# Kernel tuning notes

Measured on AMD Instinct MI355X. Metric: run time of the kernel, lower is better.

Reference implementation:

```python
import jax, jax.numpy as jnp
import numpy as np

NUM_HEADS = 16
NUM_KV_HEADS = 8
HEAD_DIM = 128
HIDDEN = 2048
Q_SIZE = NUM_HEADS * HEAD_DIM          # 2048
KV_SIZE = NUM_KV_HEADS * HEAD_DIM      # 1024
SCALING = 256.0 ** -0.5                # query_pre_attn_scalar ** -0.5
EPS = 1e-6
BATCH = 8
ENC_LEN = 512                          # encoder_len_per_req
Q_LEN = 2048                           # sum of extend_seq_lens (8 * 256)
KV_LEN = BATCH * ENC_LEN               # 4096


def _rms_norm(x, w):
    # Gemma3RMSNorm: fp32 compute, scale by (1 + weight)
    xf = x.astype(jnp.float32)
    xf = xf * jax.lax.rsqrt(jnp.mean(xf * xf, axis=-1, keepdims=True) + EPS)
    return (xf * (1.0 + w.astype(jnp.float32))).astype(x.dtype)


def setup_inputs() -> dict:
    key = jax.random.key(0)
    k1, k2, k3 = jax.random.split(key, 3)
    return {
        "hidden_states": jax.random.normal(k1, (Q_LEN, HIDDEN), jnp.float32),
        "encoder_hidden_states": jax.random.normal(k2, (KV_LEN, HIDDEN), jnp.float32),
        "w_qkv": jax.random.normal(k3, (Q_SIZE + 2 * KV_SIZE, HIDDEN), jnp.float32) * 0.02,
        "q_norm_w": jnp.zeros((HEAD_DIM,), jnp.float32),
        "k_norm_w": jnp.zeros((HEAD_DIM,), jnp.float32),
        "seq_lens": jnp.full((BATCH,), Q_LEN // BATCH, jnp.int32),  # extend_seq_lens per request
    }


def reference(hidden_states, encoder_hidden_states, w_qkv, q_norm_w, k_norm_w, seq_lens):
    # decoder side: only q is used
    qkv_dec = hidden_states @ w_qkv.T                     # [q_len, 4096]
    q = qkv_dec[:, :Q_SIZE].reshape(Q_LEN, NUM_HEADS, HEAD_DIM)
    q = _rms_norm(q, q_norm_w) * SCALING

    # encoder side: only k, v are used
    qkv_enc = encoder_hidden_states @ w_qkv.T             # [kv_len, 4096]
    k = qkv_enc[:, Q_SIZE:Q_SIZE + KV_SIZE].reshape(KV_LEN, NUM_KV_HEADS, HEAD_DIM)
    v = qkv_enc[:, Q_SIZE + KV_SIZE:].reshape(KV_LEN, NUM_KV_HEADS, HEAD_DIM)
    k = _rms_norm(k, k_norm_w)

    # GQA: repeat each kv head n_rep times (consecutively, matching expand+reshape)
    n_rep = NUM_HEADS // NUM_KV_HEADS
    k = jnp.repeat(k, n_rep, axis=1)                      # [kv_len, H, D]
    v = jnp.repeat(v, n_rep, axis=1)

    # scores per head: [H, q_len, kv_len]
    scores = jnp.einsum('qhd,khd->hqk', q, k)

    # ragged block-diagonal mask: query token i belongs to request r iff
    # cumsum(seq_lens)[r-1] <= i < cumsum(seq_lens)[r]; kv token j -> j // ENC_LEN
    q_req = jnp.searchsorted(jnp.cumsum(seq_lens), jnp.arange(Q_LEN), side='right')
    kv_req = jnp.arange(KV_LEN) // ENC_LEN
    mask = q_req[:, None] == kv_req[None, :]              # [q_len, kv_len] bool
    scores = jnp.where(mask[None, :, :], scores, -jnp.inf)

    attn = jax.nn.softmax(scores.astype(jnp.float32), axis=-1).astype(v.dtype)
    out = jnp.einsum('hqk,khd->qhd', attn, v)             # [q_len, H, D]
    return out.reshape(Q_LEN, NUM_HEADS * HEAD_DIM)
```

## Files before the change

### kernel.cpp

```cpp
#include <hip/hip_runtime.h>

typedef __attribute__((ext_vector_type(8))) short short8;
typedef __attribute__((ext_vector_type(4))) float f32x4;

#define DEVI __device__ __forceinline__

static constexpr int HIDDEN   = 2048;
static constexpr int NHEADS   = 16;
static constexpr int NKV      = 8;
static constexpr int HDIM     = 128;
static constexpr int QLEN     = 2048;
static constexpr int KVLEN    = 4096;
static constexpr int ENCLEN   = 512;
static constexpr int NREQ     = 8;
static constexpr float SCALING = 0.0625f;
static constexpr float EPS     = 1e-6f;

DEVI unsigned short f2bf(float f) {
  unsigned int b = __float_as_uint(f);
  b += 0x7FFFu + ((b >> 16) & 1u);
  return (unsigned short)(b >> 16);
}

DEVI void g2l16(const void* g, void* l) {
  __builtin_amdgcn_global_load_lds(
      (const __attribute__((address_space(1))) void*)g,
      (__attribute__((address_space(3))) void*)l, 16, 0, 0);
}

__global__ __launch_bounds__(256) void cvt_all(const float* __restrict__ h,
                                               const float* __restrict__ e,
                                               const float* __restrict__ w,
                                               unsigned short* __restrict__ hb,
                                               unsigned short* __restrict__ eb,
                                               unsigned short* __restrict__ wb) {
  constexpr long S1 = (long)2048 * 2048, S2 = (long)4096 * 2048;
  long i = ((long)blockIdx.x * 256 + threadIdx.x) * 8;
  const float* src;
  unsigned short* dst;
  if (i < S1)           { src = h + i;            dst = hb + i; }
  else if (i < S1 + S2) { src = e + (i - S1);     dst = eb + (i - S1); }
  else                  { src = w + (i - S1 - S2); dst = wb + (i - S1 - S2); }
  float4 a = *(const float4*)src;
  float4 b = *(const float4*)(src + 4);
  short8 o;
  o[0] = (short)f2bf(a.x); o[1] = (short)f2bf(a.y);
  o[2] = (short)f2bf(a.z); o[3] = (short)f2bf(a.w);
  o[4] = (short)f2bf(b.x); o[5] = (short)f2bf(b.y);
  o[6] = (short)f2bf(b.z); o[7] = (short)f2bf(b.w);
  *(short8*)dst = o;
}


#define LGKM0 { asm volatile("s_waitcnt lgkmcnt(0)" ::: "memory"); __builtin_amdgcn_sched_barrier(0); }
#define VM8   { asm volatile("s_waitcnt vmcnt(8)" ::: "memory"); __builtin_amdgcn_sched_barrier(0); }
#define VM4   { asm volatile("s_waitcnt vmcnt(4)" ::: "memory"); __builtin_amdgcn_sched_barrier(0); }
#define VM0   { asm volatile("s_waitcnt vmcnt(0)" ::: "memory"); __builtin_amdgcn_sched_barrier(0); }
#define SBAR  __builtin_amdgcn_s_barrier()

DEVI short8 rdfrag(const char* unit, int row, int lg) {
  int L = row >> 1;
  int g = ((row & 1) << 2) + lg;
  return *(const short8*)(unit + L * 128 + ((g ^ (L & 7)) << 4));
}

__global__ __launch_bounds__(512, 2) void gemm_qkv8(
    const unsigned short* __restrict__ Adec, const unsigned short* __restrict__ Aenc,
    const unsigned short* __restrict__ Bw,
    const float* __restrict__ q_nw, const float* __restrict__ k_nw,
    unsigned short* __restrict__ q_bf, unsigned short* __restrict__ k_bf,
    unsigned short* __restrict__ v_t) {
  extern __shared__ char lds[];
  const int K = 2048, NT = 32;

  int flat = blockIdx.y * 8 + blockIdx.x;
  int swz = (flat & 7) * 24 + (flat >> 3);
  int bx = swz & 7, by = swz >> 3;

  const unsigned short* A;
  int bm0;
  if (by < 8) { A = Adec; bm0 = by * 256; }
  else        { A = Aenc; bm0 = (by - 8) * 256; }
  const unsigned short* Bp = Bw + (by < 8 ? 0 : (size_t)2048 * 2048);
  const int bn0 = bx * 256;

  const int tid = threadIdx.x, lane = tid & 63, wave = tid >> 6;
  const int lr = lane & 15, lg = lane >> 4;
  const int wr = wave >> 2, wc = wave & 3;
  const int bq = (wc & 1) * 64;

#define SLOT(kt, kk) ((((kt) << 1) | (kk)) & 3)
#define AUs(s, h) (lds + ((((s) << 1) | (h)) << 13))
#define BUs(s, h) (lds + 65536 + ((((s) << 1) | (h)) << 13))

  const int sB = tid * 16;
  const int sL = sB >> 7, sgp = (sB >> 4) & 7;
  const int sg = sgp ^ (sL & 7);
  const int st_row = sL * 2 + (sg >> 2);
  const int st_col = (sg & 3) * 8;
  const size_t a0off = (size_t)(bm0 + st_row) * K + st_col;
  const size_t a1off = a0off + (size_t)128 * K;
  const size_t b0off = (size_t)(bn0 + st_row) * K + st_col;
  const size_t b1off = b0off + (size_t)128 * K;

#define STG(srcp, ubase) g2l16((srcp), (ubase) + sB)
#define STG4(kt, kk)                                                \
  {                                                                 \
    const size_t kc = (size_t)(kt) * 64 + (kk) * 32;                \
    const int s_ = SLOT(kt, kk);                                    \
    STG(A + a0off + kc, AUs(s_, 0));  STG(A + a1off + kc, AUs(s_, 1)); \
    STG(Bp + b0off + kc, BUs(s_, 0)); STG(Bp + b1off + kc, BUs(s_, 1)); \
  }

  f32x4 acc[8][4] = {};
  short8 a[4], b[4];

#define DS_A(s, mq)                                                 \
  {                                                                 \
    const char* u = AUs(s, wr);                                     \
    _Pragma("unroll") for (int m = 0; m < 4; ++m)                   \
        a[m] = rdfrag(u, (mq)*64 + m * 16 + lr, lg);                \
  }
#define DS_B(s)                                                     \
  {                                                                 \
    const char* u = BUs(s, wc >> 1);                                \
    _Pragma("unroll") for (int n = 0; n < 4; ++n)                   \
        b[n] = rdfrag(u, bq + n * 16 + lr, lg);                     \
  }
#define MFMA16(mq)                                                  \
  {                                                                 \
    __builtin_amdgcn_s_setprio(1);                                  \
    _Pragma("unroll") for (int m = 0; m < 4; ++m)                   \
        _Pragma("unroll") for (int n = 0; n < 4; ++n)               \
            acc[(mq)*4 + m][n] = __builtin_amdgcn_mfma_f32_16x16x32_bf16( \
                a[m], b[n], acc[(mq)*4 + m][n], 0, 0, 0);           \
    __builtin_amdgcn_s_setprio(0);                                  \
  }

  STG4(0, 0); STG4(0, 1); STG4(1, 0);
  VM8; SBAR;

  for (int kt = 0; kt < NT - 2; ++kt) {
    const int s0 = SLOT(kt, 0), s1 = SLOT(kt, 1);
    DS_A(s0, 0); DS_B(s0); STG4(kt + 1, 1); LGKM0; MFMA16(0); SBAR;
    DS_A(s0, 1);                            LGKM0; MFMA16(1); VM8; SBAR;
    DS_A(s1, 0); DS_B(s1); STG4(kt + 2, 0); LGKM0; MFMA16(0); SBAR;
    DS_A(s1, 1);                            LGKM0; MFMA16(1); VM8; SBAR;
  }
  {
    const int s0 = SLOT(NT - 2, 0), s1 = SLOT(NT - 2, 1);
    DS_A(s0, 0); DS_B(s0); STG4(NT - 1, 1); LGKM0; MFMA16(0); SBAR;
    DS_A(s0, 1);                            LGKM0; MFMA16(1); VM8; SBAR;
    DS_A(s1, 0); DS_B(s1);                  LGKM0; MFMA16(0); SBAR;
    DS_A(s1, 1);                            LGKM0; MFMA16(1); VM4; SBAR;
  }
  {
    const int s0 = SLOT(NT - 1, 0), s1 = SLOT(NT - 1, 1);
    DS_A(s0, 0); DS_B(s0); LGKM0; MFMA16(0); SBAR;
    DS_A(s0, 1);           LGKM0; MFMA16(1); VM0; SBAR;
    DS_A(s1, 0); DS_B(s1); LGKM0; MFMA16(0); SBAR;
    DS_A(s1, 1);           LGKM0; MFMA16(1);
  }

  const int btype = (by < 8) ? 0 : (bx < 4 ? 1 : 2);
  const int tokbase0 = (by < 8 ? by : by - 8) * 256;

  if (btype < 2) {
    float* Lf = (float*)lds;
    const float* wnorm = (btype == 0) ? q_nw : k_nw;
    const float fscale = (btype == 0) ? SCALING : 1.0f;
    unsigned short* dst = (btype == 0) ? q_bf : k_bf;
    const size_t LEN = (btype == 0) ? (size_t)QLEN : (size_t)KVLEN;
    const int dloc = lr * 8;
    float wv[8];
#pragma unroll
    for (int j = 0; j < 8; ++j) wv[j] = 1.0f + wnorm[dloc + j];

#pragma unroll
    for (int q = 0; q < 4; ++q) {
      SBAR;
      if (wr == (q >> 1)) {
        const int amb = (q & 1) * 4;
#pragma unroll
        for (int am2 = 0; am2 < 4; ++am2)
#pragma unroll
          for (int n = 0; n < 4; ++n)
#pragma unroll
            for (int r = 0; r < 4; ++r)
              Lf[(am2 * 16 + lg * 4 + r) * 260 + wc * 64 + n * 16 + lr] =
                  acc[amb + am2][n][r];
      }
      SBAR;
#pragma unroll
      for (int it = 0; it < 4; ++it) {
        int pair = it * 32 + wave * 4 + (lane >> 4);
        int row = pair >> 1, hh = pair & 1;
        const float* src = &Lf[row * 260 + hh * 128 + dloc];
        f32x4 x0 = *(const f32x4*)src;
        f32x4 x1 = *(const f32x4*)(src + 4);
        float ssq = x0[0]*x0[0] + x0[1]*x0[1] + x0[2]*x0[2] + x0[3]*x0[3] +
                    x1[0]*x1[0] + x1[1]*x1[1] + x1[2]*x1[2] + x1[3]*x1[3];
#pragma unroll
        for (int m = 8; m >= 1; m >>= 1) ssq += __shfl_xor(ssq, m);
        float sc = rsqrtf(ssq * (1.0f / 128.0f) + EPS) * fscale;
        short8 o;
        o[0] = (short)f2bf(x0[0] * sc * wv[0]); o[1] = (short)f2bf(x0[1] * sc * wv[1]);
        o[2] = (short)f2bf(x0[2] * sc * wv[2]); o[3] = (short)f2bf(x0[3] * sc * wv[3]);
        o[4] = (short)f2bf(x1[0] * sc * wv[4]); o[5] = (short)f2bf(x1[1] * sc * wv[5]);
        o[6] = (short)f2bf(x1[2] * sc * wv[6]); o[7] = (short)f2bf(x1[3] * sc * wv[7]);
        int tok = tokbase0 + q * 64 + row;
        int hd = 2 * bx + hh;
        *(short8*)&dst[((size_t)hd * LEN + tok) * 128 + dloc] = o;
      }
    }
  } else {
    float* Lv = (float*)lds;
#pragma unroll
    for (int q = 0; q < 4; ++q) {
      SBAR;
      if (wr == (q >> 1)) {
        const int amb = (q & 1) * 4;
#pragma unroll
        for (int am2 = 0; am2 < 4; ++am2)
#pragma unroll
          for (int n = 0; n < 4; ++n)
            *(f32x4*)&Lv[(wc * 64 + n * 16 + lr) * 68 + am2 * 16 + lg * 4] =
                acc[amb + am2][n];
      }
      SBAR;
      int d = tid >> 1, th = tid & 1;
      const float* src = &Lv[d * 68 + th * 32];
      int kh = (bx - 4) * 2 + (d >> 7);
      int tok = tokbase0 + q * 64 + th * 32;
      unsigned short* vp = &v_t[((size_t)kh * 128 + (d & 127)) * KVLEN + tok];
#pragma unroll
      for (int j = 0; j < 4; ++j) {
        f32x4 v0 = *(const f32x4*)(src + j * 8);
        f32x4 v1 = *(const f32x4*)(src + j * 8 + 4);
        short8 o;
        o[0] = (short)f2bf(v0[0]); o[1] = (short)f2bf(v0[1]);
        o[2] = (short)f2bf(v0[2]); o[3] = (short)f2bf(v0[3]);
        o[4] = (short)f2bf(v1[0]); o[5] = (short)f2bf(v1[1]);
        o[6] = (short)f2bf(v1[2]); o[7] = (short)f2bf(v1[3]);
        *(short8*)(vp + j * 8) = o;
      }
    }
  }
#undef SLOT
#undef AUs
#undef BUs
#undef STG
#undef STG4
#undef DS_A
#undef DS_B
#undef MFMA16
}

__global__ __launch_bounds__(256, 4) void attn_kernel(
    const unsigned short* __restrict__ qb,
    const unsigned short* __restrict__ kb,
    const unsigned short* __restrict__ vt,
    const int* __restrict__ seq_lens,
    float* __restrict__ out) {
  __shared__ __align__(16) unsigned short Ks[64 * 128];
  __shared__ __align__(16) unsigned short Vs[128 * 64];
  __shared__ __align__(16) unsigned short Ps[64 * 64];

  const int h = blockIdx.y;
  const int t0 = blockIdx.x * 64;
  int req = 0, qs = 0;
#pragma unroll 1
  while (req < NREQ - 1 && qs + seq_lens[req] <= t0) { qs += seq_lens[req]; ++req; }
  const int slen = seq_lens[req];
  const int rows = min(64, qs + slen - t0);
  if (rows <= 0) return;
  const int qbase = t0;

  const int tid = threadIdx.x, lane = tid & 63, wave = tid >> 6;
  const int lr = lane & 15, lg = lane >> 4;
  const int m0w = wave * 16;
  const int kh = h >> 1;
  const int kv0 = req * ENCLEN;

  short8 a_q[4];
  {
    int qr = qbase + min(m0w + lr, rows - 1);
    const unsigned short* qp = qb + ((size_t)h * QLEN + qr) * 128 + lg * 8;
#pragma unroll
    for (int ks = 0; ks < 4; ++ks) a_q[ks] = *(const short8*)(qp + ks * 32);
  }

  f32x4 acc[8] = {};
  float mrow[4], lsum[4];
#pragma unroll
  for (int r = 0; r < 4; ++r) { mrow[r] = -1e30f; lsum[r] = 0.f; }

  for (int c = 0; c < 8; ++c) {
#pragma unroll
    for (int i = 0; i < 4; ++i) {
      int idx = i * 256 + tid;
      int row = idx >> 4, slot = idx & 15;
      g2l16(kb + ((size_t)kh * KVLEN + kv0 + c * 64 + row) * 128 + ((slot ^ (row & 15)) << 3),
            &Ks[idx * 8]);
    }
#pragma unroll
    for (int i = 0; i < 4; ++i) {
      int idx = i * 256 + tid;
      int row = idx >> 3, slot = idx & 7;
      g2l16(vt + ((size_t)kh * 128 + row) * KVLEN + kv0 + c * 64 + ((slot ^ (row & 7)) << 3),
            &Vs[idx * 8]);
    }
    __syncthreads();

    f32x4 s[4] = {};
#pragma unroll
    for (int ks = 0; ks < 4; ++ks) {
      short8 bk[4];
#pragma unroll
      for (int n = 0; n < 4; ++n) {
        int row = n * 16 + lr;
        bk[n] = *(const short8*)&Ks[row * 128 + (((ks * 4 + lg) ^ (row & 15)) << 3)];
      }
#pragma unroll
      for (int n = 0; n < 4; ++n)
        s[n] = __builtin_amdgcn_mfma_f32_16x16x32_bf16(a_q[ks], bk[n], s[n], 0, 0, 0);
    }

#pragma unroll
    for (int r = 0; r < 4; ++r) {
      float mx = fmaxf(fmaxf(s[0][r], s[1][r]), fmaxf(s[2][r], s[3][r]));
#pragma unroll
      for (int msk = 8; msk >= 1; msk >>= 1) mx = fmaxf(mx, __shfl_xor(mx, msk));
      float mnew = fmaxf(mrow[r], mx);
      float al = __expf(mrow[r] - mnew);
      mrow[r] = mnew;
      float rs = 0.f;
#pragma unroll
      for (int n = 0; n < 4; ++n) {
        float p = __expf(s[n][r] - mnew);
        s[n][r] = p;
        rs += p;
      }
#pragma unroll
      for (int msk = 8; msk >= 1; msk >>= 1) rs += __shfl_xor(rs, msk);
      lsum[r] = lsum[r] * al + rs;
#pragma unroll
      for (int n2 = 0; n2 < 8; ++n2) acc[n2][r] *= al;
    }

#pragma unroll
    for (int n = 0; n < 4; ++n)
#pragma unroll
      for (int r = 0; r < 4; ++r) {
        int row = m0w + lg * 4 + r;
        int col = n * 16 + lr;
        Ps[row * 64 + (col ^ ((row & 7) << 3))] = f2bf(s[n][r]);
      }
    asm volatile("s_waitcnt lgkmcnt(0)" ::: "memory");
    __builtin_amdgcn_sched_barrier(0);

#pragma unroll
    for (int ks = 0; ks < 2; ++ks) {
      int prow = m0w + lr;
      short8 pa = *(const short8*)&Ps[prow * 64 + (((ks * 4 + lg) ^ (prow & 7)) << 3)];
#pragma unroll
      for (int n2 = 0; n2 < 8; ++n2) {
        int row = n2 * 16 + lr;
        short8 bv = *(const short8*)&Vs[row * 64 + (((ks * 4 + lg) ^ (row & 7)) << 3)];
        acc[n2] = __builtin_amdgcn_mfma_f32_16x16x32_bf16(pa, bv, acc[n2], 0, 0, 0);
      }
    }
    __syncthreads();
  }

  float inv[4];
#pragma unroll
  for (int r = 0; r < 4; ++r) inv[r] = 1.0f / lsum[r];
#pragma unroll
  for (int n2 = 0; n2 < 8; ++n2)
#pragma unroll
    for (int r = 0; r < 4; ++r) acc[n2][r] *= inv[r];

  constexpr int OFS = 132;
  float* Of = (float*)Ks;
#pragma unroll
  for (int n2 = 0; n2 < 8; ++n2)
#pragma unroll
    for (int r = 0; r < 4; ++r)
      Of[(m0w + lg * 4 + r) * OFS + n2 * 16 + lr] = acc[n2][r];
  __syncthreads();
#pragma unroll
  for (int p = 0; p < 8; ++p) {
    int idx = p * 256 + tid;
    int row = idx >> 5, c4 = (idx & 31) * 4;
    if (row < rows) {
      f32x4 v = *(const f32x4*)&Of[row * OFS + c4];
      *(f32x4*)&out[(size_t)(qbase + row) * 2048 + h * 128 + c4] = v;
    }
  }
}

extern "C" void kernel_launch(void* const* d_in, const int* in_sizes, int n_in,
                              void* d_out, int out_size, void* d_ws, size_t ws_size,
                              hipStream_t stream) {
  const float* hidden = (const float*)d_in[0];
  const float* enc    = (const float*)d_in[1];
  const float* w_qkv  = (const float*)d_in[2];
  const float* q_nw   = (const float*)d_in[3];
  const float* k_nw   = (const float*)d_in[4];
  const int*   slens  = (const int*)d_in[5];
  float* out = (float*)d_out;

  char* ws = (char*)d_ws;
  unsigned short* h_bf = (unsigned short*)(ws + 0);
  unsigned short* e_bf = (unsigned short*)(ws + 8388608);
  unsigned short* w_bf = (unsigned short*)(ws + 25165824);
  unsigned short* q_bf = (unsigned short*)(ws + 41943040);
  unsigned short* k_bf = (unsigned short*)(ws + 50331648);
  unsigned short* v_t  = (unsigned short*)(ws + 58720256);

  static bool attr_set = false;
  if (!attr_set) {
    hipFuncSetAttribute((const void*)gemm_qkv8,
                        hipFuncAttributeMaxDynamicSharedMemorySize, 131072);
    attr_set = true;
  }

  cvt_all<<<10240, 256, 0, stream>>>(hidden, enc, w_qkv, h_bf, e_bf, w_bf);

  gemm_qkv8<<<dim3(8, 24), 512, 131072, stream>>>(h_bf, e_bf, w_bf, q_nw, k_nw,
                                                  q_bf, k_bf, v_t);

  attn_kernel<<<dim3(32, 16), 256, 0, stream>>>(q_bf, k_bf, v_t, slens, out);
}
```

Before: 116.2 us.

## Double-buffer LDS fragment registers to overlap ds_reads with MFMA in QKV GEMM

Restructures the QKV GEMM main loop so the LDS fragment loads for the next MFMA group go into alternate register sets (aE/aO, bX/bY) while the current group's MFMAs run. The explicit lgkmcnt(0) waits and sched barriers are removed, leaving the compiler to insert LDS waits. The goal is to hide LDS read latency behind matrix math. In exchange it uses more VGPRs under a 512-thread, 2-block launch bound, which may cause spills, and the vmcnt waits now sit before the LDS reads.

```diff
diff --git a/kernel.cpp b/kernel.cpp
--- a/kernel.cpp
+++ b/kernel.cpp
@@ -52,10 +52,9 @@
 }
 
 
-#define LGKM0 { asm volatile("s_waitcnt lgkmcnt(0)" ::: "memory"); __builtin_amdgcn_sched_barrier(0); }
-#define VM8   { asm volatile("s_waitcnt vmcnt(8)" ::: "memory"); __builtin_amdgcn_sched_barrier(0); }
-#define VM4   { asm volatile("s_waitcnt vmcnt(4)" ::: "memory"); __builtin_amdgcn_sched_barrier(0); }
-#define VM0   { asm volatile("s_waitcnt vmcnt(0)" ::: "memory"); __builtin_amdgcn_sched_barrier(0); }
+#define VM8   { asm volatile("s_waitcnt vmcnt(8)" ::: "memory"); }
+#define VM4   { asm volatile("s_waitcnt vmcnt(4)" ::: "memory"); }
+#define VM0   { asm volatile("s_waitcnt vmcnt(0)" ::: "memory"); }
 #define SBAR  __builtin_amdgcn_s_barrier()
 
 DEVI short8 rdfrag(const char* unit, int row, int lg) {
@@ -113,53 +112,58 @@
   }
 
   f32x4 acc[8][4] = {};
-  short8 a[4], b[4];
-
-#define DS_A(s, mq)                                                 \
+  short8 aE[4], aO[4], bX[4], bY[4];
+
+#define LDA(dst, s, mq)                                             \
   {                                                                 \
     const char* u = AUs(s, wr);                                     \
     _Pragma("unroll") for (int m = 0; m < 4; ++m)                   \
-        a[m] = rdfrag(u, (mq)*64 + m * 16 + lr, lg);                \
-  }
-#define DS_B(s)                                                     \
+        dst[m] = rdfrag(u, (mq)*64 + m * 16 + lr, lg);              \
+  }
+#define LDB(dst, s)                                                 \
   {                                                                 \
     const char* u = BUs(s, wc >> 1);                                \
     _Pragma("unroll") for (int n = 0; n < 4; ++n)                   \
-        b[n] = rdfrag(u, bq + n * 16 + lr, lg);                     \
-  }
-#define MFMA16(mq)                                                  \
+        dst[n] = rdfrag(u, bq + n * 16 + lr, lg);                   \
+  }
+#define MM(mq, aS, bS)                                              \
   {                                                                 \
     __builtin_amdgcn_s_setprio(1);                                  \
     _Pragma("unroll") for (int m = 0; m < 4; ++m)                   \
         _Pragma("unroll") for (int n = 0; n < 4; ++n)               \
             acc[(mq)*4 + m][n] = __builtin_amdgcn_mfma_f32_16x16x32_bf16( \
-                a[m], b[n], acc[(mq)*4 + m][n], 0, 0, 0);           \
+                aS[m], bS[n], acc[(mq)*4 + m][n], 0, 0, 0);         \
     __builtin_amdgcn_s_setprio(0);                                  \
   }
 
   STG4(0, 0); STG4(0, 1); STG4(1, 0);
   VM8; SBAR;
+  LDA(aE, SLOT(0, 0), 0);
+  LDB(bX, SLOT(0, 0));
 
   for (int kt = 0; kt < NT - 2; ++kt) {
     const int s0 = SLOT(kt, 0), s1 = SLOT(kt, 1);
-    DS_A(s0, 0); DS_B(s0); STG4(kt + 1, 1); LGKM0; MFMA16(0); SBAR;
-    DS_A(s0, 1);                            LGKM0; MFMA16(1); VM8; SBAR;
-    DS_A(s1, 0); DS_B(s1); STG4(kt + 2, 0); LGKM0; MFMA16(0); SBAR;
-    DS_A(s1, 1);                            LGKM0; MFMA16(1); VM8; SBAR;
+    VM8; LDA(aO, s0, 1); STG4(kt + 1, 1);            MM(0, aE, bX); SBAR;
+    VM8; LDA(aE, s1, 0); LDB(bY, s1);                MM(1, aO, bX); SBAR;
+    VM8; LDA(aO, s1, 1); STG4(kt + 2, 0);            MM(0, aE, bY); SBAR;
+    VM8; LDA(aE, SLOT(kt + 1, 0), 0);
+         LDB(bX, SLOT(kt + 1, 0));                   MM(1, aO, bY); SBAR;
   }
   {
-    const int s0 = SLOT(NT - 2, 0), s1 = SLOT(NT - 2, 1);
-    DS_A(s0, 0); DS_B(s0); STG4(NT - 1, 1); LGKM0; MFMA16(0); SBAR;
-    DS_A(s0, 1);                            LGKM0; MFMA16(1); VM8; SBAR;
-    DS_A(s1, 0); DS_B(s1);                  LGKM0; MFMA16(0); SBAR;
-    DS_A(s1, 1);                            LGKM0; MFMA16(1); VM4; SBAR;
+    const int kt = NT - 2;
+    const int s0 = SLOT(kt, 0), s1 = SLOT(kt, 1);
+    VM8; LDA(aO, s0, 1); STG4(NT - 1, 1);            MM(0, aE, bX); SBAR;
+    VM8; LDA(aE, s1, 0); LDB(bY, s1);                MM(1, aO, bX); SBAR;
+    VM8; LDA(aO, s1, 1);                             MM(0, aE, bY); SBAR;
+    VM4; LDA(aE, SLOT(NT - 1, 0), 0);
+         LDB(bX, SLOT(NT - 1, 0));                   MM(1, aO, bY); SBAR;
   }
   {
     const int s0 = SLOT(NT - 1, 0), s1 = SLOT(NT - 1, 1);
-    DS_A(s0, 0); DS_B(s0); LGKM0; MFMA16(0); SBAR;
-    DS_A(s0, 1);           LGKM0; MFMA16(1); VM0; SBAR;
-    DS_A(s1, 0); DS_B(s1); LGKM0; MFMA16(0); SBAR;
-    DS_A(s1, 1);           LGKM0; MFMA16(1);
+    VM4; LDA(aO, s0, 1);                             MM(0, aE, bX); SBAR;
+    VM0; LDA(aE, s1, 0); LDB(bY, s1);                MM(1, aO, bX); SBAR;
+         LDA(aO, s1, 1);                             MM(0, aE, bY); SBAR;
+                                                     MM(1, aO, bY);
   }
 
   const int btype = (by < 8) ? 0 : (bx < 4 ? 1 : 2);
@@ -251,9 +255,9 @@
 #undef BUs
 #undef STG
 #undef STG4
-#undef DS_A
-#undef DS_B
-#undef MFMA16
+#undef LDA
+#undef LDB
+#undef MM
 }
 
 __global__ __launch_bounds__(256, 4) void attn_kernel(
```

Result: no change. 114.8 us (-1.2%).

## Restructure GEMM into 3-stage ring pipeline and double-buffer attention K/V loads

Applied to the files above, without the earlier changes.

The QKV GEMM main loop drops the 4-slot, two-half-step schedule with explicit lgkm/vm waits. It becomes a simpler 3-buffer ring over 32-wide k-steps, with one barrier per step and prefetch two steps ahead. The attention kernel now double-buffers the K and V tiles in shared memory, so the next chunk's global-to-LDS loads overlap the current chunk's compute, and one barrier per iteration is removed. The cost is more LDS in attention (72KB), which may cut occupancy from 4 blocks per CU. The GEMM also loses its fine-grained wait placement and now does twice as many barrier steps.

```diff
diff --git a/kernel.cpp b/kernel.cpp
--- a/kernel.cpp
+++ b/kernel.cpp
@@ -52,10 +52,6 @@
 }
 
 
-#define LGKM0 { asm volatile("s_waitcnt lgkmcnt(0)" ::: "memory"); __builtin_amdgcn_sched_barrier(0); }
-#define VM8   { asm volatile("s_waitcnt vmcnt(8)" ::: "memory"); __builtin_amdgcn_sched_barrier(0); }
-#define VM4   { asm volatile("s_waitcnt vmcnt(4)" ::: "memory"); __builtin_amdgcn_sched_barrier(0); }
-#define VM0   { asm volatile("s_waitcnt vmcnt(0)" ::: "memory"); __builtin_amdgcn_sched_barrier(0); }
 #define SBAR  __builtin_amdgcn_s_barrier()
 
 DEVI short8 rdfrag(const char* unit, int row, int lg) {
@@ -71,7 +67,7 @@
     unsigned short* __restrict__ q_bf, unsigned short* __restrict__ k_bf,
     unsigned short* __restrict__ v_t) {
   extern __shared__ char lds[];
-  const int K = 2048, NT = 32;
+  const int K = 2048, NST = 64;
 
   int flat = blockIdx.y * 8 + blockIdx.x;
   int swz = (flat & 7) * 24 + (flat >> 3);
@@ -88,10 +84,6 @@
   const int lr = lane & 15, lg = lane >> 4;
   const int wr = wave >> 2, wc = wave & 3;
   const int bq = (wc & 1) * 64;
-
-#define SLOT(kt, kk) ((((kt) << 1) | (kk)) & 3)
-#define AUs(s, h) (lds + ((((s) << 1) | (h)) << 13))
-#define BUs(s, h) (lds + 65536 + ((((s) << 1) | (h)) << 13))
 
   const int sB = tid * 16;
   const int sL = sB >> 7, sgp = (sB >> 4) & 7;
@@ -103,63 +95,61 @@
   const size_t b0off = (size_t)(bn0 + st_row) * K + st_col;
   const size_t b1off = b0off + (size_t)128 * K;
 
-#define STG(srcp, ubase) g2l16((srcp), (ubase) + sB)
-#define STG4(kt, kk)                                                \
-  {                                                                 \
-    const size_t kc = (size_t)(kt) * 64 + (kk) * 32;                \
-    const int s_ = SLOT(kt, kk);                                    \
-    STG(A + a0off + kc, AUs(s_, 0));  STG(A + a1off + kc, AUs(s_, 1)); \
-    STG(Bp + b0off + kc, BUs(s_, 0)); STG(Bp + b1off + kc, BUs(s_, 1)); \
+#define STG4(t)                                                       \
+  {                                                                   \
+    const size_t kc = (size_t)(t) * 32;                               \
+    char* base = lds + ((t) % 3) * 32768;                             \
+    g2l16(A + a0off + kc,  base + sB);                                \
+    g2l16(A + a1off + kc,  base + 8192 + sB);                         \
+    g2l16(Bp + b0off + kc, base + 16384 + sB);                        \
+    g2l16(Bp + b1off + kc, base + 24576 + sB);                        \
   }
 
   f32x4 acc[8][4] = {};
-  short8 a[4], b[4];
-
-#define DS_A(s, mq)                                                 \
-  {                                                                 \
-    const char* u = AUs(s, wr);                                     \
-    _Pragma("unroll") for (int m = 0; m < 4; ++m)                   \
-        a[m] = rdfrag(u, (mq)*64 + m * 16 + lr, lg);                \
-  }
-#define DS_B(s)                                                     \
-  {                                                                 \
-    const char* u = BUs(s, wc >> 1);                                \
-    _Pragma("unroll") for (int n = 0; n < 4; ++n)                   \
-        b[n] = rdfrag(u, bq + n * 16 + lr, lg);                     \
-  }
-#define MFMA16(mq)                                                  \
-  {                                                                 \
-    __builtin_amdgcn_s_setprio(1);                                  \
-    _Pragma("unroll") for (int m = 0; m < 4; ++m)                   \
-        _Pragma("unroll") for (int n = 0; n < 4; ++n)               \
+
+#define MM(mq, aS, bS)                                                \
+  {                                                                   \
+    __builtin_amdgcn_s_setprio(1);                                    \
+    _Pragma("unroll") for (int m = 0; m < 4; ++m)                     \
+        _Pragma("unroll") for (int n = 0; n < 4; ++n)                 \
             acc[(mq)*4 + m][n] = __builtin_amdgcn_mfma_f32_16x16x32_bf16( \
-                a[m], b[n], acc[(mq)*4 + m][n], 0, 0, 0);           \
-    __builtin_amdgcn_s_setprio(0);                                  \
-  }
-
-  STG4(0, 0); STG4(0, 1); STG4(1, 0);
-  VM8; SBAR;
-
-  for (int kt = 0; kt < NT - 2; ++kt) {
-    const int s0 = SLOT(kt, 0), s1 = SLOT(kt, 1);
-    DS_A(s0, 0); DS_B(s0); STG4(kt + 1, 1); LGKM0; MFMA16(0); SBAR;
-    DS_A(s0, 1);                            LGKM0; MFMA16(1); VM8; SBAR;
-    DS_A(s1, 0); DS_B(s1); STG4(kt + 2, 0); LGKM0; MFMA16(0); SBAR;
-    DS_A(s1, 1);                            LGKM0; MFMA16(1); VM8; SBAR;
+                aS[m], bS[n], acc[(mq)*4 + m][n], 0, 0, 0);           \
+    __builtin_amdgcn_s_setprio(0);                                    \
+  }
+
+  STG4(0); STG4(1);
+
+#pragma unroll 3
+  for (int t = 0; t < NST - 1; ++t) {
+    asm volatile("s_waitcnt vmcnt(4)" ::: "memory");
+    SBAR;
+    const char* ua = lds + (t % 3) * 32768 + wr * 8192;
+    const char* ub = lds + (t % 3) * 32768 + 16384 + ((wc >> 1) << 13);
+    short8 a0[4], b0[4], a1[4];
+#pragma unroll
+    for (int m = 0; m < 4; ++m) a0[m] = rdfrag(ua, m * 16 + lr, lg);
+#pragma unroll
+    for (int n = 0; n < 4; ++n) b0[n] = rdfrag(ub, bq + n * 16 + lr, lg);
+    if (t < NST - 2) STG4(t + 2);
+    MM(0, a0, b0);
+#pragma unroll
+    for (int m = 0; m < 4; ++m) a1[m] = rdfrag(ua, 64 + m * 16 + lr, lg);
+    MM(1, a1, b0);
   }
   {
-    const int s0 = SLOT(NT - 2, 0), s1 = SLOT(NT - 2, 1);
-    DS_A(s0, 0); DS_B(s0); STG4(NT - 1, 1); LGKM0; MFMA16(0); SBAR;
-    DS_A(s0, 1);                            LGKM0; MFMA16(1); VM8; SBAR;
-    DS_A(s1, 0); DS_B(s1);                  LGKM0; MFMA16(0); SBAR;
-    DS_A(s1, 1);                            LGKM0; MFMA16(1); VM4; SBAR;
-  }
-  {
-    const int s0 = SLOT(NT - 1, 0), s1 = SLOT(NT - 1, 1);
-    DS_A(s0, 0); DS_B(s0); LGKM0; MFMA16(0); SBAR;
-    DS_A(s0, 1);           LGKM0; MFMA16(1); VM0; SBAR;
-    DS_A(s1, 0); DS_B(s1); LGKM0; MFMA16(0); SBAR;
-    DS_A(s1, 1);           LGKM0; MFMA16(1);
+    asm volatile("s_waitcnt vmcnt(0)" ::: "memory");
+    SBAR;
+    const char* ua = lds + ((NST - 1) % 3) * 32768 + wr * 8192;
+    const char* ub = lds + ((NST - 1) % 3) * 32768 + 16384 + ((wc >> 1) << 13);
+    short8 a0[4], b0[4], a1[4];
+#pragma unroll
+    for (int m = 0; m < 4; ++m) a0[m] = rdfrag(ua, m * 16 + lr, lg);
+#pragma unroll
+    for (int n = 0; n < 4; ++n) b0[n] = rdfrag(ub, bq + n * 16 + lr, lg);
+    MM(0, a0, b0);
+#pragma unroll
+    for (int m = 0; m < 4; ++m) a1[m] = rdfrag(ua, 64 + m * 16 + lr, lg);
+    MM(1, a1, b0);
   }
 
   const int btype = (by < 8) ? 0 : (bx < 4 ? 1 : 2);
@@ -246,14 +236,8 @@
       }
     }
   }
-#undef SLOT
-#undef AUs
-#undef BUs
-#undef STG
 #undef STG4
-#undef DS_A
-#undef DS_B
-#undef MFMA16
+#undef MM
 }
 
 __global__ __launch_bounds__(256, 4) void attn_kernel(
@@ -262,9 +246,7 @@
     const unsigned short* __restrict__ vt,
     const int* __restrict__ seq_lens,
     float* __restrict__ out) {
-  __shared__ __align__(16) unsigned short Ks[64 * 128];
-  __shared__ __align__(16) unsigned short Vs[128 * 64];
-  __shared__ __align__(16) unsigned short Ps[64 * 64];
+  __shared__ __align__(16) char smem[73728];
 
   const int h = blockIdx.y;
   const int t0 = blockIdx.x * 64;
@@ -282,6 +264,25 @@
   const int kh = h >> 1;
   const int kv0 = req * ENCLEN;
 
+#define STAGE_K(c, db)                                                        \
+  _Pragma("unroll") for (int i = 0; i < 4; ++i) {                             \
+    int idx = i * 256 + tid;                                                  \
+    int row = idx >> 4, slot = idx & 15;                                      \
+    g2l16(kb + ((size_t)kh * KVLEN + kv0 + (c) * 64 + row) * 128 +            \
+              ((slot ^ (row & 15)) << 3),                                     \
+          smem + (db) * 16384 + idx * 16);                                    \
+  }
+#define STAGE_V(c, db)                                                        \
+  _Pragma("unroll") for (int i = 0; i < 4; ++i) {                             \
+    int idx = i * 256 + tid;                                                  \
+    int row = idx >> 3, slot = idx & 7;                                       \
+    g2l16(vt + ((size_t)kh * 128 + row) * KVLEN + kv0 + (c) * 64 +            \
+              ((slot ^ (row & 7)) << 3),                                      \
+          smem + 32768 + (db) * 16384 + idx * 16);                            \
+  }
+
+  unsigned short* Ps = (unsigned short*)(smem + 65536);
+
   short8 a_q[4];
   {
     int qr = qbase + min(m0w + lr, rows - 1);
@@ -295,22 +296,16 @@
 #pragma unroll
   for (int r = 0; r < 4; ++r) { mrow[r] = -1e30f; lsum[r] = 0.f; }
 
+  STAGE_K(0, 0); STAGE_V(0, 0);
+
+  int cb = 0;
+#pragma unroll 1
   for (int c = 0; c < 8; ++c) {
-#pragma unroll
-    for (int i = 0; i < 4; ++i) {
-      int idx = i * 256 + tid;
-      int row = idx >> 4, slot = idx & 15;
-      g2l16(kb + ((size_t)kh * KVLEN + kv0 + c * 64 + row) * 128 + ((slot ^ (row & 15)) << 3),
-            &Ks[idx * 8]);
-    }
-#pragma unroll
-    for (int i = 0; i < 4; ++i) {
-      int idx = i * 256 + tid;
-      int row = idx >> 3, slot = idx & 7;
-      g2l16(vt + ((size_t)kh * 128 + row) * KVLEN + kv0 + c * 64 + ((slot ^ (row & 7)) << 3),
-            &Vs[idx * 8]);
-    }
+    asm volatile("s_waitcnt vmcnt(0)" ::: "memory");
     __syncthreads();
+    if (c < 7) { STAGE_K(c + 1, cb ^ 1); STAGE_V(c + 1, cb ^ 1); }
+    const unsigned short* Kb = (const unsigned short*)(smem + cb * 16384);
+    const unsigned short* Vb = (const unsigned short*)(smem + 32768 + cb * 16384);
 
     f32x4 s[4] = {};
 #pragma unroll
@@ -319,7 +314,7 @@
 #pragma unroll
       for (int n = 0; n < 4; ++n) {
         int row = n * 16 + lr;
-        bk[n] = *(const short8*)&Ks[row * 128 + (((ks * 4 + lg) ^ (row & 15)) << 3)];
+        bk[n] = *(const short8*)&Kb[row * 128 + (((ks * 4 + lg) ^ (row & 15)) << 3)];
       }
 #pragma unroll
       for (int n = 0; n < 4; ++n)
@@ -366,12 +361,13 @@
 #pragma unroll
       for (int n2 = 0; n2 < 8; ++n2) {
         int row = n2 * 16 + lr;
-        short8 bv = *(const short8*)&Vs[row * 64 + (((ks * 4 + lg) ^ (row & 7)) << 3)];
+        short8 bv = *(const short8*)&Vb[row * 64 + (((ks * 4 + lg) ^ (row & 7)) << 3)];
         acc[n2] = __builtin_amdgcn_mfma_f32_16x16x32_bf16(pa, bv, acc[n2], 0, 0, 0);
       }
     }
-    __syncthreads();
-  }
+    cb ^= 1;
+  }
+  __syncthreads();
 
   float inv[4];
 #pragma unroll
@@ -382,7 +378,7 @@
     for (int r = 0; r < 4; ++r) acc[n2][r] *= inv[r];
 
   constexpr int OFS = 132;
-  float* Of = (float*)Ks;
+  float* Of = (float*)smem;
 #pragma unroll
   for (int n2 = 0; n2 < 8; ++n2)
 #pragma unroll
@@ -398,6 +394,8 @@
       *(f32x4*)&out[(size_t)(qbase + row) * 2048 + h * 128 + c4] = v;
     }
   }
+#undef STAGE_K
+#undef STAGE_V
 }
 
 extern "C" void kernel_launch(void* const* d_in, const int* in_sizes, int n_in,
```

New measurement: 102.2 us (median of 3 runs). -12.0%, faster.
